# Performance work log

Measured on AMD Instinct MI355X. Metric: run time of the kernel, lower is better.

## Reference

```python
import jax, jax.numpy as jnp
import numpy as np

DIM = 1024
NUM_HEADS = 16
HEAD_DIM = DIM // NUM_HEADS
SCALE = HEAD_DIM ** -0.5
HIDDEN = int(DIM * 1.0)


def setup_inputs() -> dict:
    key = jax.random.key(0)
    ks = jax.random.split(key, 11)
    s = 0.02
    return {
        "x":  jax.random.normal(ks[0], (2, 2048, DIM), jnp.float32),
        "Wq": jax.random.normal(ks[1], (DIM, DIM), jnp.float32) * s,
        "bq": jnp.zeros((DIM,), jnp.float32),
        "Wk": jax.random.normal(ks[2], (DIM, DIM), jnp.float32) * s,
        "bk": jnp.zeros((DIM,), jnp.float32),
        "Wv": jax.random.normal(ks[3], (DIM, DIM), jnp.float32) * s,
        "bv": jnp.zeros((DIM,), jnp.float32),
        "W1": jax.random.normal(ks[4], (HIDDEN, DIM), jnp.float32) * s,
        "b1": jnp.zeros((HIDDEN,), jnp.float32),
        "W2": jax.random.normal(ks[5], (DIM, HIDDEN), jnp.float32) * s,
        "b2": jnp.zeros((DIM,), jnp.float32),
    }


def _split_heads(t, B, S):
    # [B,S,C] -> [B,H,S,hd]
    return t.reshape(B, S, NUM_HEADS, HEAD_DIM).transpose(0, 2, 1, 3)


def reference(x, Wq, bq, Wk, bk, Wv, bv, W1, b1, W2, b2):
    B, S, C = x.shape
    q = _split_heads(x @ Wq.T + bq, B, S) * SCALE
    k = _split_heads(x @ Wk.T + bk, B, S)
    v = _split_heads(x @ Wv.T + bv, B, S)
    # softmax-free bilinear attention, scores in float32 (matches .float())
    attn = jnp.einsum('bhqd,bhkd->bhqk', q.astype(jnp.float32), k.astype(jnp.float32))
    out = jnp.einsum('bhqk,bhkd->bhqd', attn, v)  # [B,H,S,hd]
    out = out.transpose(0, 2, 1, 3).reshape(B, S, C)
    h = jax.nn.gelu(out @ W1.T + b1, approximate=False)
    mlp = h @ W2.T + b2
    return x + out + mlp
```

## Files before the change

### kernel.cpp

```cpp
#include <hip/hip_runtime.h>
#include <math.h>

#define DIM    1024
#define BATCH  2
#define SEQ    2048
#define NHEAD  16
#define HDIM   64
#define MROWS  (BATCH*SEQ)
#define NSPLIT 8

typedef unsigned short u16;
typedef __attribute__((ext_vector_type(8))) short  s16x8;
typedef __attribute__((ext_vector_type(4))) float  f32x4;

__device__ __forceinline__ float bf2f(u16 h) {
    unsigned u = ((unsigned)h) << 16; float f; __builtin_memcpy(&f, &u, 4); return f;
}
__device__ __forceinline__ u16 f2bf(float f) {
    unsigned u; __builtin_memcpy(&u, &f, 4);
    u += 0x7FFFu + ((u >> 16) & 1u);
    return (u16)(u >> 16);
}

__global__ __launch_bounds__(256)
void pack_all(const float* __restrict__ x,
              const float* __restrict__ Wq, const float* __restrict__ Wk,
              const float* __restrict__ Wv, const float* __restrict__ W1,
              const float* __restrict__ W2,
              u16* __restrict__ xb, u16* __restrict__ Wqb, u16* __restrict__ Wkb,
              u16* __restrict__ Wvb, u16* __restrict__ W1b, u16* __restrict__ W2b)
{
    const int bid = blockIdx.x;
    const float* src; u16* dst; int i;
    if (bid < 4096) { src = x; dst = xb; i = bid * 256 + threadIdx.x; }
    else {
        const int w = (bid - 4096) >> 10;
        const int lb = (bid - 4096) & 1023;
        src = (w == 0) ? Wq : (w == 1) ? Wk : (w == 2) ? Wv : (w == 3) ? W1 : W2;
        dst = (w == 0) ? Wqb : (w == 1) ? Wkb : (w == 2) ? Wvb : (w == 3) ? W1b : W2b;
        i = lb * 256 + threadIdx.x;
    }
    float4 v = ((const float4*)src)[i];
    ushort4 o = { f2bf(v.x), f2bf(v.y), f2bf(v.z), f2bf(v.w) };
    ((ushort4*)dst)[i] = o;
}

__device__ __forceinline__ void gemm_core_pf128(const u16* __restrict__ Ab,
                                                const u16* __restrict__ Bb,
                                                u16* As, u16* Bs,
                                                int tid, f32x4 acc[4][4])
{
    const int w = tid >> 6, l = tid & 63;
    const int wm = (w >> 1) * 64, wn = (w & 1) * 64;
    const int lr = l & 15, kq = l >> 4;
    const int row = tid >> 2, cg8 = (tid & 3) * 8;

    const u16* a0 = Ab + (size_t)row * DIM + cg8;
    const u16* a1 = Ab + (size_t)(64 + row) * DIM + cg8;
    const u16* b0 = Bb + (size_t)row * DIM + cg8;
    const u16* b1 = Bb + (size_t)(64 + row) * DIM + cg8;

    uint4 pa0 = *(const uint4*)a0, pa1 = *(const uint4*)a1;
    uint4 pb0 = *(const uint4*)b0, pb1 = *(const uint4*)b1;
    *(uint4*)(As + tid * 8) = pa0;  *(uint4*)(As + 2048 + tid * 8) = pa1;
    *(uint4*)(Bs + tid * 8) = pb0;  *(uint4*)(Bs + 2048 + tid * 8) = pb1;

    const int NIT = DIM / 32;
    for (int it = 0; it < NIT; ++it) {
        u16* Ac = As + (it & 1) * 4096;
        u16* Bc = Bs + (it & 1) * 4096;
        __syncthreads();
        if (it + 1 < NIT) {
            const int k = (it + 1) * 32;
            pa0 = *(const uint4*)(a0 + k); pa1 = *(const uint4*)(a1 + k);
            pb0 = *(const uint4*)(b0 + k); pb1 = *(const uint4*)(b1 + k);
        }
        s16x8 af[4], bfr[4];
        #pragma unroll
        for (int i = 0; i < 4; ++i)
            af[i]  = *(const s16x8*)(Ac + (wm + i * 16 + lr) * 32 + kq * 8);
        #pragma unroll
        for (int j = 0; j < 4; ++j)
            bfr[j] = *(const s16x8*)(Bc + (wn + j * 16 + lr) * 32 + kq * 8);
        #pragma unroll
        for (int i = 0; i < 4; ++i)
            #pragma unroll
            for (int j = 0; j < 4; ++j)
                acc[i][j] = __builtin_amdgcn_mfma_f32_16x16x32_bf16(af[i], bfr[j], acc[i][j], 0, 0, 0);
        if (it + 1 < NIT) {
            u16* An = As + ((it + 1) & 1) * 4096;
            u16* Bn = Bs + ((it + 1) & 1) * 4096;
            *(uint4*)(An + tid * 8) = pa0;  *(uint4*)(An + 2048 + tid * 8) = pa1;
            *(uint4*)(Bn + tid * 8) = pb0;  *(uint4*)(Bn + 2048 + tid * 8) = pb1;
        }
    }
}

__device__ __forceinline__ void gemm_core_pf64(const u16* __restrict__ Ab,
                                               const u16* __restrict__ Bb,
                                               u16* As , u16* Bs ,
                                               int tid, f32x4 acc[2][4])
{
    const int w  = tid >> 6, l = tid & 63;
    const int wm = (w >> 1) * 32, wn = (w & 1) * 64;
    const int lr = l & 15, kq = l >> 4;
    const int row = tid >> 2, cg8 = (tid & 3) * 8;

    const u16* a0 = Ab + (size_t)row * DIM + cg8;
    const u16* b0 = Bb + (size_t)row * DIM + cg8;
    const u16* b1 = Bb + (size_t)(64 + row) * DIM + cg8;

    uint4 pa  = *(const uint4*)a0;
    uint4 pb0 = *(const uint4*)b0, pb1 = *(const uint4*)b1;
    *(uint4*)(As + tid * 8) = pa;
    *(uint4*)(Bs + tid * 8) = pb0; *(uint4*)(Bs + 2048 + tid * 8) = pb1;

    const int NIT = DIM / 32;
    for (int it = 0; it < NIT; ++it) {
        u16* Ac = As + (it & 1) * 2048;
        u16* Bc = Bs + (it & 1) * 4096;
        __syncthreads();
        if (it + 1 < NIT) {
            const int k = (it + 1) * 32;
            pa  = *(const uint4*)(a0 + k);
            pb0 = *(const uint4*)(b0 + k); pb1 = *(const uint4*)(b1 + k);
        }
        s16x8 af[2], bfr[4];
        #pragma unroll
        for (int i = 0; i < 2; ++i)
            af[i]  = *(const s16x8*)(Ac + (wm + i * 16 + lr) * 32 + kq * 8);
        #pragma unroll
        for (int j = 0; j < 4; ++j)
            bfr[j] = *(const s16x8*)(Bc + (wn + j * 16 + lr) * 32 + kq * 8);
        #pragma unroll
        for (int i = 0; i < 2; ++i)
            #pragma unroll
            for (int j = 0; j < 4; ++j)
                acc[i][j] = __builtin_amdgcn_mfma_f32_16x16x32_bf16(af[i], bfr[j], acc[i][j], 0, 0, 0);
        if (it + 1 < NIT) {
            u16* An = As + ((it + 1) & 1) * 2048;
            u16* Bn = Bs + ((it + 1) & 1) * 4096;
            *(uint4*)(An + tid * 8) = pa;
            *(uint4*)(Bn + tid * 8) = pb0; *(uint4*)(Bn + 2048 + tid * 8) = pb1;
        }
    }
}

__global__ __launch_bounds__(256)
void qkv_gemm(const u16* __restrict__ xb,
              const u16* __restrict__ Wq, const u16* __restrict__ Wk, const u16* __restrict__ Wv,
              const float* __restrict__ bq, const float* __restrict__ bk, const float* __restrict__ bv,
              u16* __restrict__ qo, u16* __restrict__ ko, u16* __restrict__ vo)
{
    __shared__ u16 As[2 * 4096];
    __shared__ u16 Bs[2 * 4096];
    const int tid = threadIdx.x;
    const int m0  = blockIdx.x * 128;
    const int sel = blockIdx.y >> 3;
    const int n0  = (blockIdx.y & 7) * 128;
    const u16*   B    = (sel == 0) ? Wq : (sel == 1) ? Wk : Wv;
    const float* bias = (sel == 0) ? bq : (sel == 1) ? bk : bv;
    u16*         C    = (sel == 0) ? qo : (sel == 1) ? ko : vo;
    const float scale = (sel == 0) ? 0.125f : 1.0f;

    f32x4 acc[4][4];
    #pragma unroll
    for (int i = 0; i < 4; ++i)
        #pragma unroll
        for (int j = 0; j < 4; ++j) acc[i][j] = (f32x4){0.f, 0.f, 0.f, 0.f};

    gemm_core_pf128(xb + (size_t)m0 * DIM, B + (size_t)n0 * DIM, As, Bs, tid, acc);

    const int w = tid >> 6, l = tid & 63;
    const int wm = (w >> 1) * 64, wn = (w & 1) * 64;
    const int er = l >> 4, ec = l & 15;
    #pragma unroll
    for (int j = 0; j < 4; ++j) {
        const int n = n0 + wn + j * 16 + ec;
        const float bb = bias[n];
        #pragma unroll
        for (int i = 0; i < 4; ++i)
            #pragma unroll
            for (int r = 0; r < 4; ++r) {
                const int m = m0 + wm + i * 16 + er * 4 + r;
                C[(size_t)m * DIM + n] = f2bf((acc[i][j][r] + bb) * scale);
            }
    }
}

__global__ __launch_bounds__(256)
void gemm_bf16(const u16* __restrict__ A, const u16* __restrict__ B,
               const float* __restrict__ bias,
               u16* __restrict__ Cb, float* __restrict__ Cf,
               const float* __restrict__ rx, const u16* __restrict__ rattn,
               int mode)
{
    __shared__ u16 As[2 * 2048];
    __shared__ u16 Bs[2 * 4096];
    const int tid = threadIdx.x;
    const int m0 = blockIdx.x * 64, n0 = blockIdx.y * 128;

    f32x4 acc[2][4];
    #pragma unroll
    for (int i = 0; i < 2; ++i)
        #pragma unroll
        for (int j = 0; j < 4; ++j) acc[i][j] = (f32x4){0.f, 0.f, 0.f, 0.f};

    gemm_core_pf64(A + (size_t)m0 * DIM, B + (size_t)n0 * DIM, As, Bs, tid, acc);

    const int w = tid >> 6, l = tid & 63;
    const int wm = (w >> 1) * 32, wn = (w & 1) * 64;
    const int er = l >> 4, ec = l & 15;
    #pragma unroll
    for (int j = 0; j < 4; ++j) {
        const int n = n0 + wn + j * 16 + ec;
        const float bb = bias[n];
        #pragma unroll
        for (int i = 0; i < 2; ++i)
            #pragma unroll
            for (int r = 0; r < 4; ++r) {
                const int m = m0 + wm + i * 16 + er * 4 + r;
                const size_t idx = (size_t)m * DIM + n;
                float v = acc[i][j][r] + bb;
                if (mode == 1) {
                    v = 0.5f * v * (1.0f + erff(v * 0.70710678118654752f));
                    Cb[idx] = f2bf(v);
                } else {
                    Cf[idx] = v + rx[idx] + bf2f(rattn[idx]);
                }
            }
    }
}

__global__ __launch_bounds__(256)
void ktv_mfma(const u16* __restrict__ Kb, const u16* __restrict__ Vb,
              float* __restrict__ part)
{
    __shared__ u16 Kt[64 * 264];
    __shared__ u16 Vt[64 * 264];
    const int tid = threadIdx.x;
    const int bh = blockIdx.x & 31;
    const int sp = blockIdx.x >> 5;
    const int b = bh >> 4, h = bh & 15;
    const size_t base = (size_t)b * SEQ * DIM + (size_t)h * HDIM + (size_t)sp * 256 * DIM;

    const int dg = (tid & 15) * 4;
    #pragma unroll
    for (int pass = 0; pass < 16; ++pass) {
        const int s = (tid >> 4) + 16 * pass;
        ushort4 kv = *(const ushort4*)(Kb + base + (size_t)s * DIM + dg);
        ushort4 vv = *(const ushort4*)(Vb + base + (size_t)s * DIM + dg);
        Kt[(dg + 0) * 264 + s] = kv.x; Kt[(dg + 1) * 264 + s] = kv.y;
        Kt[(dg + 2) * 264 + s] = kv.z; Kt[(dg + 3) * 264 + s] = kv.w;
        Vt[(dg + 0) * 264 + s] = vv.x; Vt[(dg + 1) * 264 + s] = vv.y;
        Vt[(dg + 2) * 264 + s] = vv.z; Vt[(dg + 3) * 264 + s] = vv.w;
    }
    __syncthreads();

    const int w = tid >> 6, l = tid & 63;
    const int lr = l & 15, kq = l >> 4;
    f32x4 acc[4];
    #pragma unroll
    for (int j = 0; j < 4; ++j) acc[j] = (f32x4){0.f, 0.f, 0.f, 0.f};

    for (int k0 = 0; k0 < 256; k0 += 32) {
        s16x8 af = *(const s16x8*)(Kt + (w * 16 + lr) * 264 + k0 + kq * 8);
        #pragma unroll
        for (int j = 0; j < 4; ++j) {
            s16x8 bf = *(const s16x8*)(Vt + (j * 16 + lr) * 264 + k0 + kq * 8);
            acc[j] = __builtin_amdgcn_mfma_f32_16x16x32_bf16(af, bf, acc[j], 0, 0, 0);
        }
    }

    float* dst = part + ((size_t)sp * 32 + bh) * (HDIM * HDIM);
    const int er = l >> 4, ec = l & 15;
    #pragma unroll
    for (int j = 0; j < 4; ++j)
        #pragma unroll
        for (int r = 0; r < 4; ++r)
            dst[(w * 16 + er * 4 + r) * HDIM + j * 16 + ec] = acc[j][r];
}

__global__ __launch_bounds__(256)
void qktv_kernel(const u16* __restrict__ Qb, const float* __restrict__ part,
                 u16* __restrict__ attnb)
{
    __shared__ float KV[HDIM * HDIM];
    __shared__ u16 Qs[128 * 68];
    const int tid = threadIdx.x;
    const int h  = blockIdx.x;
    const int mt = blockIdx.y;
    const int row0 = mt * 128;
    const int b = row0 >> 11;
    const int bh = b * NHEAD + h;

    for (int i = tid; i < HDIM * HDIM; i += 256) {
        float s = 0.f;
        #pragma unroll
        for (int sp = 0; sp < NSPLIT; ++sp)
            s += part[((size_t)sp * 32 + bh) * (HDIM * HDIM) + i];
        KV[i] = s;
    }
    const int dg = (tid & 15) * 4;
    #pragma unroll
    for (int pass = 0; pass < 8; ++pass) {
        const int r = (tid >> 4) + 16 * pass;
        ushort4 q = *(const ushort4*)(Qb + (size_t)(row0 + r) * DIM + h * HDIM + dg);
        *(ushort4*)(Qs + r * 68 + dg) = q;
    }
    __syncthreads();

    const int tr = tid >> 3, tc = tid & 7;
    const int r0 = tr * 4, c0 = tc * 8;
    float acc[4][8] = {};
    for (int d = 0; d < HDIM; ++d) {
        float4 ka  = *(const float4*)&KV[d * HDIM + c0];
        float4 kb2 = *(const float4*)&KV[d * HDIM + c0 + 4];
        const float* k8a = (const float*)&ka;
        const float* k8b = (const float*)&kb2;
        float qv[4];
        #pragma unroll
        for (int i = 0; i < 4; ++i) qv[i] = bf2f(Qs[(r0 + i) * 68 + d]);
        #pragma unroll
        for (int i = 0; i < 4; ++i)
            #pragma unroll
            for (int j = 0; j < 4; ++j) {
                acc[i][j]     += qv[i] * k8a[j];
                acc[i][j + 4] += qv[i] * k8b[j];
            }
    }
    #pragma unroll
    for (int i = 0; i < 4; ++i) {
        u16* dst = attnb + (size_t)(row0 + r0 + i) * DIM + h * HDIM + c0;
        ushort4 o0 = { f2bf(acc[i][0]), f2bf(acc[i][1]), f2bf(acc[i][2]), f2bf(acc[i][3]) };
        ushort4 o1 = { f2bf(acc[i][4]), f2bf(acc[i][5]), f2bf(acc[i][6]), f2bf(acc[i][7]) };
        *(ushort4*)(dst)     = o0;
        *(ushort4*)(dst + 4) = o1;
    }
}

extern "C" void kernel_launch(void* const* d_in, const int* in_sizes, int n_in,
                              void* d_out, int out_size, void* d_ws, size_t ws_size,
                              hipStream_t stream)
{
    const float* x  = (const float*)d_in[0];
    const float* Wq = (const float*)d_in[1];
    const float* bq = (const float*)d_in[2];
    const float* Wk = (const float*)d_in[3];
    const float* bk = (const float*)d_in[4];
    const float* Wv = (const float*)d_in[5];
    const float* bv = (const float*)d_in[6];
    const float* W1 = (const float*)d_in[7];
    const float* b1 = (const float*)d_in[8];
    const float* W2 = (const float*)d_in[9];
    const float* b2 = (const float*)d_in[10];
    float* out = (float*)d_out;

    char* ws = (char*)d_ws;
    const size_t MB = 1u << 20;
    u16* xb   = (u16*)(ws);
    u16* Wqb  = (u16*)(ws +  8 * MB);
    u16* Wkb  = (u16*)(ws + 10 * MB);
    u16* Wvb  = (u16*)(ws + 12 * MB);
    u16* W1b  = (u16*)(ws + 14 * MB);
    u16* W2b  = (u16*)(ws + 16 * MB);
    u16* qb   = (u16*)(ws + 18 * MB);
    u16* kb   = (u16*)(ws + 26 * MB);
    u16* vb   = (u16*)(ws + 34 * MB);
    float* part = (float*)(ws + 42 * MB);
    u16* attnb = kb;
    u16* h1b   = vb;

    pack_all<<<4096 + 5 * 1024, 256, 0, stream>>>(x, Wq, Wk, Wv, W1, W2,
                                                  xb, Wqb, Wkb, Wvb, W1b, W2b);

    qkv_gemm<<<dim3(32, 24), 256, 0, stream>>>(xb, Wqb, Wkb, Wvb, bq, bk, bv, qb, kb, vb);

    ktv_mfma<<<NSPLIT * 32, 256, 0, stream>>>(kb, vb, part);
    qktv_kernel<<<dim3(NHEAD, MROWS / 128), 256, 0, stream>>>(qb, part, attnb);

    gemm_bf16<<<dim3(64, 8), 256, 0, stream>>>(attnb, W1b, b1, h1b, nullptr, nullptr, nullptr, 1);
    gemm_bf16<<<dim3(64, 8), 256, 0, stream>>>(h1b, W2b, b2, nullptr, out, x, attnb, 2);
}
```

Before: 203.2 us.

## Use direct global-to-LDS loads with swizzled layout and LDS-staged coalesced epilogues

Replaces the register-staged global loads plus LDS stores in both GEMM cores with buffer global_load_lds direct-to-LDS transfers, using an XOR-swizzled LDS layout to avoid bank conflicts on fragment reads. Epilogues of the QKV and MLP GEMMs now write results into shared memory and then emit coalesced 16-byte row stores (and vectorized residual reads) instead of scattered 2/4-byte stores. This aims to cut VGPR pressure, load latency and uncoalesced write traffic, but it relies on implicit ordering of async LDS loads before the barrier and adds extra syncs in the epilogue.

```diff
diff --git a/kernel.cpp b/kernel.cpp
--- a/kernel.cpp
+++ b/kernel.cpp
@@ -20,6 +20,12 @@
     unsigned u; __builtin_memcpy(&u, &f, 4);
     u += 0x7FFFu + ((u >> 16) & 1u);
     return (u16)(u >> 16);
+}
+
+__device__ __forceinline__ void glds16(const u16* g, u16* l) {
+    __builtin_amdgcn_global_load_lds(
+        (const __attribute__((address_space(1))) void*)g,
+        (__attribute__((address_space(3))) void*)l, 16, 0, 0);
 }
 
 __global__ __launch_bounds__(256)
@@ -53,46 +59,39 @@
     const int w = tid >> 6, l = tid & 63;
     const int wm = (w >> 1) * 64, wn = (w & 1) * 64;
     const int lr = l & 15, kq = l >> 4;
-    const int row = tid >> 2, cg8 = (tid & 3) * 8;
-
-    const u16* a0 = Ab + (size_t)row * DIM + cg8;
-    const u16* a1 = Ab + (size_t)(64 + row) * DIM + cg8;
-    const u16* b0 = Bb + (size_t)row * DIM + cg8;
-    const u16* b1 = Bb + (size_t)(64 + row) * DIM + cg8;
-
-    uint4 pa0 = *(const uint4*)a0, pa1 = *(const uint4*)a1;
-    uint4 pb0 = *(const uint4*)b0, pb1 = *(const uint4*)b1;
-    *(uint4*)(As + tid * 8) = pa0;  *(uint4*)(As + 2048 + tid * 8) = pa1;
-    *(uint4*)(Bs + tid * 8) = pb0;  *(uint4*)(Bs + 2048 + tid * 8) = pb1;
-
+    const int swl = l ^ (w << 1);
+    const u16* gA = Ab + (size_t)swl * DIM + w * 8;
+    const u16* gB = Bb + (size_t)swl * DIM + w * 8;
+    const int rdA = kq * 1024 + wm * 8 + ((lr ^ (kq << 1)) << 3);
+    const int rdB = kq * 1024 + wn * 8 + ((lr ^ (kq << 1)) << 3);
+
+    {
+        u16* a = As + w * 1024; u16* b = Bs + w * 1024;
+        glds16(gA, a); glds16(gA + 64 * DIM, a + 512);
+        glds16(gB, b); glds16(gB + 64 * DIM, b + 512);
+    }
     const int NIT = DIM / 32;
     for (int it = 0; it < NIT; ++it) {
-        u16* Ac = As + (it & 1) * 4096;
-        u16* Bc = Bs + (it & 1) * 4096;
         __syncthreads();
         if (it + 1 < NIT) {
             const int k = (it + 1) * 32;
-            pa0 = *(const uint4*)(a0 + k); pa1 = *(const uint4*)(a1 + k);
-            pb0 = *(const uint4*)(b0 + k); pb1 = *(const uint4*)(b1 + k);
-        }
+            u16* a = As + ((it + 1) & 1) * 4096 + w * 1024;
+            u16* b = Bs + ((it + 1) & 1) * 4096 + w * 1024;
+            glds16(gA + k, a); glds16(gA + k + 64 * DIM, a + 512);
+            glds16(gB + k, b); glds16(gB + k + 64 * DIM, b + 512);
+        }
+        const u16* Ac = As + (it & 1) * 4096;
+        const u16* Bc = Bs + (it & 1) * 4096;
         s16x8 af[4], bfr[4];
         #pragma unroll
-        for (int i = 0; i < 4; ++i)
-            af[i]  = *(const s16x8*)(Ac + (wm + i * 16 + lr) * 32 + kq * 8);
-        #pragma unroll
-        for (int j = 0; j < 4; ++j)
-            bfr[j] = *(const s16x8*)(Bc + (wn + j * 16 + lr) * 32 + kq * 8);
+        for (int i = 0; i < 4; ++i) af[i]  = *(const s16x8*)(Ac + rdA + i * 128);
+        #pragma unroll
+        for (int j = 0; j < 4; ++j) bfr[j] = *(const s16x8*)(Bc + rdB + j * 128);
         #pragma unroll
         for (int i = 0; i < 4; ++i)
             #pragma unroll
             for (int j = 0; j < 4; ++j)
                 acc[i][j] = __builtin_amdgcn_mfma_f32_16x16x32_bf16(af[i], bfr[j], acc[i][j], 0, 0, 0);
-        if (it + 1 < NIT) {
-            u16* An = As + ((it + 1) & 1) * 4096;
-            u16* Bn = Bs + ((it + 1) & 1) * 4096;
-            *(uint4*)(An + tid * 8) = pa0;  *(uint4*)(An + 2048 + tid * 8) = pa1;
-            *(uint4*)(Bn + tid * 8) = pb0;  *(uint4*)(Bn + 2048 + tid * 8) = pb1;
-        }
     }
 }
 
@@ -104,45 +103,39 @@
     const int w  = tid >> 6, l = tid & 63;
     const int wm = (w >> 1) * 32, wn = (w & 1) * 64;
     const int lr = l & 15, kq = l >> 4;
-    const int row = tid >> 2, cg8 = (tid & 3) * 8;
-
-    const u16* a0 = Ab + (size_t)row * DIM + cg8;
-    const u16* b0 = Bb + (size_t)row * DIM + cg8;
-    const u16* b1 = Bb + (size_t)(64 + row) * DIM + cg8;
-
-    uint4 pa  = *(const uint4*)a0;
-    uint4 pb0 = *(const uint4*)b0, pb1 = *(const uint4*)b1;
-    *(uint4*)(As + tid * 8) = pa;
-    *(uint4*)(Bs + tid * 8) = pb0; *(uint4*)(Bs + 2048 + tid * 8) = pb1;
-
+    const int swl = l ^ (w << 1);
+    const u16* gA = Ab + (size_t)swl * DIM + w * 8;
+    const u16* gB = Bb + (size_t)swl * DIM + w * 8;
+    const int rdA = kq * 512  + wm * 8 + ((lr ^ (kq << 1)) << 3);
+    const int rdB = kq * 1024 + wn * 8 + ((lr ^ (kq << 1)) << 3);
+
+    {
+        u16* a = As + w * 512; u16* b = Bs + w * 1024;
+        glds16(gA, a);
+        glds16(gB, b); glds16(gB + 64 * DIM, b + 512);
+    }
     const int NIT = DIM / 32;
     for (int it = 0; it < NIT; ++it) {
-        u16* Ac = As + (it & 1) * 2048;
-        u16* Bc = Bs + (it & 1) * 4096;
         __syncthreads();
         if (it + 1 < NIT) {
             const int k = (it + 1) * 32;
-            pa  = *(const uint4*)(a0 + k);
-            pb0 = *(const uint4*)(b0 + k); pb1 = *(const uint4*)(b1 + k);
-        }
+            u16* a = As + ((it + 1) & 1) * 2048 + w * 512;
+            u16* b = Bs + ((it + 1) & 1) * 4096 + w * 1024;
+            glds16(gA + k, a);
+            glds16(gB + k, b); glds16(gB + k + 64 * DIM, b + 512);
+        }
+        const u16* Ac = As + (it & 1) * 2048;
+        const u16* Bc = Bs + (it & 1) * 4096;
         s16x8 af[2], bfr[4];
         #pragma unroll
-        for (int i = 0; i < 2; ++i)
-            af[i]  = *(const s16x8*)(Ac + (wm + i * 16 + lr) * 32 + kq * 8);
-        #pragma unroll
-        for (int j = 0; j < 4; ++j)
-            bfr[j] = *(const s16x8*)(Bc + (wn + j * 16 + lr) * 32 + kq * 8);
+        for (int i = 0; i < 2; ++i) af[i]  = *(const s16x8*)(Ac + rdA + i * 128);
+        #pragma unroll
+        for (int j = 0; j < 4; ++j) bfr[j] = *(const s16x8*)(Bc + rdB + j * 128);
         #pragma unroll
         for (int i = 0; i < 2; ++i)
             #pragma unroll
             for (int j = 0; j < 4; ++j)
                 acc[i][j] = __builtin_amdgcn_mfma_f32_16x16x32_bf16(af[i], bfr[j], acc[i][j], 0, 0, 0);
-        if (it + 1 < NIT) {
-            u16* An = As + ((it + 1) & 1) * 2048;
-            u16* Bn = Bs + ((it + 1) & 1) * 4096;
-            *(uint4*)(An + tid * 8) = pa;
-            *(uint4*)(Bn + tid * 8) = pb0; *(uint4*)(Bn + 2048 + tid * 8) = pb1;
-        }
     }
 }
 
@@ -152,8 +145,7 @@
               const float* __restrict__ bq, const float* __restrict__ bk, const float* __restrict__ bv,
               u16* __restrict__ qo, u16* __restrict__ ko, u16* __restrict__ vo)
 {
-    __shared__ u16 As[2 * 4096];
-    __shared__ u16 Bs[2 * 4096];
+    __shared__ __align__(16) u16 SH[16384];
     const int tid = threadIdx.x;
     const int m0  = blockIdx.x * 128;
     const int sel = blockIdx.y >> 3;
@@ -169,22 +161,36 @@
         #pragma unroll
         for (int j = 0; j < 4; ++j) acc[i][j] = (f32x4){0.f, 0.f, 0.f, 0.f};
 
-    gemm_core_pf128(xb + (size_t)m0 * DIM, B + (size_t)n0 * DIM, As, Bs, tid, acc);
-
+    gemm_core_pf128(xb + (size_t)m0 * DIM, B + (size_t)n0 * DIM, SH, SH + 8192, tid, acc);
+
+    __syncthreads();
     const int w = tid >> 6, l = tid & 63;
     const int wm = (w >> 1) * 64, wn = (w & 1) * 64;
     const int er = l >> 4, ec = l & 15;
     #pragma unroll
     for (int j = 0; j < 4; ++j) {
-        const int n = n0 + wn + j * 16 + ec;
-        const float bb = bias[n];
+        const int colv = wn + j * 16 + ec;
+        const float bb = bias[n0 + colv];
+        const int cg = colv >> 3, cl = colv & 7;
         #pragma unroll
         for (int i = 0; i < 4; ++i)
             #pragma unroll
             for (int r = 0; r < 4; ++r) {
-                const int m = m0 + wm + i * 16 + er * 4 + r;
-                C[(size_t)m * DIM + n] = f2bf((acc[i][j][r] + bb) * scale);
+                const int row = wm + i * 16 + er * 4 + r;
+                const int g = ((row >> 2) & 3) << 1;
+                SH[row * 128 + ((cg ^ g) << 3) + cl] = f2bf((acc[i][j][r] + bb) * scale);
             }
+    }
+    __syncthreads();
+    {
+        const int cg = tid & 15, rr = tid >> 4;
+        #pragma unroll
+        for (int pass = 0; pass < 8; ++pass) {
+            const int row = rr + (pass << 4);
+            const int g = ((row >> 2) & 3) << 1;
+            uint4 v = *(const uint4*)(SH + row * 128 + ((cg ^ g) << 3));
+            *(uint4*)(C + (size_t)(m0 + row) * DIM + n0 + (cg << 3)) = v;
+        }
     }
 }
 
@@ -195,8 +201,7 @@
                const float* __restrict__ rx, const u16* __restrict__ rattn,
                int mode)
 {
-    __shared__ u16 As[2 * 2048];
-    __shared__ u16 Bs[2 * 4096];
+    __shared__ __align__(16) u16 SH[12288];
     const int tid = threadIdx.x;
     const int m0 = blockIdx.x * 64, n0 = blockIdx.y * 128;
 
@@ -206,29 +211,77 @@
         #pragma unroll
         for (int j = 0; j < 4; ++j) acc[i][j] = (f32x4){0.f, 0.f, 0.f, 0.f};
 
-    gemm_core_pf64(A + (size_t)m0 * DIM, B + (size_t)n0 * DIM, As, Bs, tid, acc);
+    gemm_core_pf64(A + (size_t)m0 * DIM, B + (size_t)n0 * DIM, SH, SH + 4096, tid, acc);
 
     const int w = tid >> 6, l = tid & 63;
     const int wm = (w >> 1) * 32, wn = (w & 1) * 64;
     const int er = l >> 4, ec = l & 15;
-    #pragma unroll
-    for (int j = 0; j < 4; ++j) {
-        const int n = n0 + wn + j * 16 + ec;
-        const float bb = bias[n];
-        #pragma unroll
-        for (int i = 0; i < 2; ++i)
-            #pragma unroll
-            for (int r = 0; r < 4; ++r) {
-                const int m = m0 + wm + i * 16 + er * 4 + r;
-                const size_t idx = (size_t)m * DIM + n;
-                float v = acc[i][j][r] + bb;
-                if (mode == 1) {
+
+    if (mode == 1) {
+        __syncthreads();
+        #pragma unroll
+        for (int j = 0; j < 4; ++j) {
+            const int colv = wn + j * 16 + ec;
+            const float bb = bias[n0 + colv];
+            const int cg = colv >> 3, cl = colv & 7;
+            #pragma unroll
+            for (int i = 0; i < 2; ++i)
+                #pragma unroll
+                for (int r = 0; r < 4; ++r) {
+                    const int row = wm + i * 16 + er * 4 + r;
+                    const int g = ((row >> 2) & 3) << 1;
+                    float v = acc[i][j][r] + bb;
                     v = 0.5f * v * (1.0f + erff(v * 0.70710678118654752f));
-                    Cb[idx] = f2bf(v);
-                } else {
-                    Cf[idx] = v + rx[idx] + bf2f(rattn[idx]);
+                    SH[row * 128 + ((cg ^ g) << 3) + cl] = f2bf(v);
+                }
+        }
+        __syncthreads();
+        const int cg = tid & 15, rr = tid >> 4;
+        #pragma unroll
+        for (int pass = 0; pass < 4; ++pass) {
+            const int row = rr + (pass << 4);
+            const int g = ((row >> 2) & 3) << 1;
+            uint4 v = *(const uint4*)(SH + row * 128 + ((cg ^ g) << 3));
+            *(uint4*)(Cb + (size_t)(m0 + row) * DIM + n0 + (cg << 3)) = v;
+        }
+    } else {
+        float* SHF = (float*)SH;
+        #pragma unroll
+        for (int h = 0; h < 2; ++h) {
+            __syncthreads();
+            if ((w >> 1) == h) {
+                #pragma unroll
+                for (int j = 0; j < 4; ++j) {
+                    const int colv = wn + j * 16 + ec;
+                    const float bb = bias[n0 + colv];
+                    const int c4 = colv >> 2, c2 = colv & 3;
+                    #pragma unroll
+                    for (int i = 0; i < 2; ++i)
+                        #pragma unroll
+                        for (int r = 0; r < 4; ++r) {
+                            const int rl = i * 16 + er * 4 + r;
+                            const int g4 = ((rl >> 2) & 1) << 2;
+                            SHF[rl * 128 + ((c4 ^ g4) << 2) + c2] = acc[i][j][r] + bb;
+                        }
                 }
             }
+            __syncthreads();
+            const int c4 = tid & 31, rr = tid >> 5;
+            #pragma unroll
+            for (int pass = 0; pass < 4; ++pass) {
+                const int rl = rr + (pass << 3);
+                const int g4 = ((rl >> 2) & 1) << 2;
+                float4 v = *(const float4*)(SHF + rl * 128 + ((c4 ^ g4) << 2));
+                const size_t idx = (size_t)(m0 + 32 * h + rl) * DIM + n0 + (c4 << 2);
+                float4 rxv = *(const float4*)(rx + idx);
+                ushort4 rav = *(const ushort4*)(rattn + idx);
+                float4 o = { v.x + rxv.x + bf2f(rav.x),
+                             v.y + rxv.y + bf2f(rav.y),
+                             v.z + rxv.z + bf2f(rav.z),
+                             v.w + rxv.w + bf2f(rav.w) };
+                *(float4*)(Cf + idx) = o;
+            }
+        }
     }
 }
 
```

New measurement: 228.7 us. 1.13x slower.
